# Optimization experiments

Hardware: AMD Instinct MI355X
Metric: run time of the kernel (lower is better)

The kernel has to match this reference:

```python
import jax, jax.numpy as jnp
import numpy as np

B, S, D_IN, HEAD_DIM = 4, 4096, 1024, 128

def setup_inputs() -> dict:
    key = jax.random.key(0)
    k1, k2, k3, k4 = jax.random.split(key, 4)
    x = jax.random.normal(k1, (B, S, D_IN), dtype=jnp.float32)
    # nn.Parameter(torch.rand(...)) -> uniform [0,1)
    W_query = jax.random.uniform(k2, (D_IN, HEAD_DIM), dtype=jnp.float32)
    W_key = jax.random.uniform(k3, (D_IN, HEAD_DIM), dtype=jnp.float32)
    W_value = jax.random.uniform(k4, (D_IN, HEAD_DIM), dtype=jnp.float32)
    return {"x": x, "W_query": W_query, "W_key": W_key, "W_value": W_value}

def reference(x, W_query, W_key, W_value):
    # x: [B,S,d_in]; W_*: [d_in,head_dim]
    queries = jnp.einsum('bsd,dh->bsh', x, W_query)
    keys = jnp.einsum('bsd,dh->bsh', x, W_key)
    values = jnp.einsum('bsd,dh->bsh', x, W_value)
    scale = 1.0 / jnp.sqrt(jnp.asarray(HEAD_DIM, dtype=x.dtype))
    attn_scores = jnp.einsum('bqh,bkh->bqk', queries, keys)  # [B,S,S]
    attn_weights = jax.nn.softmax(attn_scores * scale, axis=-1)
    context_vec = jnp.einsum('bqk,bkh->bqh', attn_weights, values)
    return context_vec
```

## Files before the change

### kernel.cpp

```cpp
#include <hip/hip_runtime.h>
#include <cstdint>

#define B_  4
#define S_  4096
#define DIN 1024
#define DH  128
#define QSCALE (0.08838834764831845f * 1.4426950408889634f)

typedef short bf16x8 __attribute__((ext_vector_type(8)));
typedef float f32x4 __attribute__((ext_vector_type(4)));
typedef unsigned short u16;
typedef unsigned int   u32;

#define MFMA16(a, b, c) __builtin_amdgcn_mfma_f32_16x16x32_bf16(a, b, c, 0, 0, 0)

#define GLOAD_LDS16(g, l) __builtin_amdgcn_global_load_lds( \
    (const __attribute__((address_space(1))) void*)(g),     \
    (__attribute__((address_space(3))) void*)(l), 16, 0, 0)

#if __has_builtin(__builtin_amdgcn_exp2f)
#define EXP2(x) __builtin_amdgcn_exp2f(x)
#else
#define EXP2(x) exp2f(x)
#endif

__device__ inline u16 bf16_rn(float f) {
    union { float f; u32 u; } v; v.f = f;
    u32 r = v.u + 0x7FFFu + ((v.u >> 16) & 1u);
    return (u16)(r >> 16);
}
__device__ inline float bf16_f(u16 h) {
    union { u32 u; float f; } v; v.u = ((u32)h) << 16; return v.f;
}
__device__ inline u32 pk2(float a, float b) {
    return (u32)bf16_rn(a) | ((u32)bf16_rn(b) << 16);
}
__device__ inline void split2(float a, float b, u32& hi, u32& lo) {
    u32 ua = __builtin_bit_cast(u32, a), ub = __builtin_bit_cast(u32, b);
    u32 ha = ua & 0xFFFF0000u, hb = ub & 0xFFFF0000u;
    hi = (ua >> 16) | hb;
    float la = a - __builtin_bit_cast(float, ha);
    float lb = b - __builtin_bit_cast(float, hb);
    lo = (u32)bf16_rn(la) | ((u32)bf16_rn(lb) << 16);
}

__global__ __launch_bounds__(256) void wconv2(
    const float* __restrict__ Wq, const float* __restrict__ Wk, const float* __restrict__ Wv,
    u16* __restrict__ wpack)
{
    int id  = blockIdx.x * 256 + threadIdx.x;
    int s   = id / 2560;
    int rem = id % 2560;
    int p   = rem >> 9;
    int gi  = rem & 511;
    int n   = gi & 127, kq2 = gi >> 7;
    const float* W = (p < 2) ? Wq : (p < 4) ? Wk : Wv;
    int k0 = 32 * s + 8 * kq2;
    u16 o[8];
    #pragma unroll
    for (int j = 0; j < 8; ++j) {
        float v = W[(size_t)(k0 + j) * DH + n];
        if (p < 2) v *= QSCALE;
        if (p == 4) {
            o[j] = bf16_rn(v);
        } else {
            u32 u = __builtin_bit_cast(u32, v);
            if ((p & 1) == 0) o[j] = (u16)(u >> 16);
            else o[j] = bf16_rn(v - __builtin_bit_cast(float, u & 0xFFFF0000u));
        }
    }
    u16* dst = wpack + (size_t)id * 8;
    *(uint4*)dst = *(uint4*)o;
}

__global__ __launch_bounds__(256, 2) void qkv_v5(
    const float* __restrict__ x, const u16* __restrict__ wpack,
    u16* __restrict__ qhi, u16* __restrict__ qlo,
    u16* __restrict__ khi, u16* __restrict__ klo, u16* __restrict__ vt)
{
    __shared__ __align__(16) char lds[65536];

    const int t    = threadIdx.x;
    const int row0 = blockIdx.x * 64;
    const int lane = t & 63, wave = t >> 6;
    const int l15  = lane & 15, g = lane >> 4;
    const int wr   = wave >> 1, wc = wave & 1;

    f32x4 accq[2][4], acck[2][4], accv[2][4];
    #pragma unroll
    for (int rt = 0; rt < 2; ++rt)
        #pragma unroll
        for (int nt = 0; nt < 4; ++nt)
            #pragma unroll
            for (int r = 0; r < 4; ++r) {
                accq[rt][nt][r] = 0.f; acck[rt][nt][r] = 0.f; accv[rt][nt][r] = 0.f;
            }

    const char* WP = (const char*)wpack;
    auto stage = [&](int bufi, int s) {
        char* d = lds + bufi * 32768;
        const char* src = WP + (size_t)s * 40960;
        #pragma unroll
        for (int c = 0; c < 8; ++c) {
            int o = t * 16 + c * 4096;
            GLOAD_LDS16(src + o, d + o);
        }
    };

    int wo_[4];
    #pragma unroll
    for (int nt = 0; nt < 4; ++nt)
        wo_[nt] = (g << 11) + ((64 * wc + 16 * nt + l15) << 4);

    const char* WV = WP + 32768;
    bf16x8 vcur[4], vnxt[4];
    #pragma unroll
    for (int nt = 0; nt < 4; ++nt)
        vcur[nt] = *(const bf16x8*)(WV + wo_[nt]);

    const float* xp0 = x + (size_t)(row0 + 32 * wr + l15) * DIN + 8 * g;
    const float* xp1 = xp0 + (size_t)16 * DIN;

    float4 ca0 = *(const float4*)(xp0);
    float4 cb0 = *(const float4*)(xp0 + 4);
    float4 ca1 = *(const float4*)(xp1);
    float4 cb1 = *(const float4*)(xp1 + 4);

    stage(0, 0);
    __syncthreads();

    int buf = 0;
    for (int s = 0; s < 32; ++s) {
        if (s < 31) stage(buf ^ 1, s + 1);

        float4 na0, nb0, na1, nb1;
        if (s < 31) {
            na0 = *(const float4*)(xp0 + 32 * (s + 1));
            nb0 = *(const float4*)(xp0 + 32 * (s + 1) + 4);
            na1 = *(const float4*)(xp1 + 32 * (s + 1));
            nb1 = *(const float4*)(xp1 + 32 * (s + 1) + 4);
            #pragma unroll
            for (int nt = 0; nt < 4; ++nt)
                vnxt[nt] = *(const bf16x8*)(WV + (size_t)(s + 1) * 40960 + wo_[nt]);
        }

        bf16x8 xh[2], xl[2];
        {
            uint4 H, L;
            split2(ca0.x, ca0.y, H.x, L.x); split2(ca0.z, ca0.w, H.y, L.y);
            split2(cb0.x, cb0.y, H.z, L.z); split2(cb0.z, cb0.w, H.w, L.w);
            xh[0] = __builtin_bit_cast(bf16x8, H);
            xl[0] = __builtin_bit_cast(bf16x8, L);
        }
        {
            uint4 H, L;
            split2(ca1.x, ca1.y, H.x, L.x); split2(ca1.z, ca1.w, H.y, L.y);
            split2(cb1.x, cb1.y, H.z, L.z); split2(cb1.z, cb1.w, H.w, L.w);
            xh[1] = __builtin_bit_cast(bf16x8, H);
            xl[1] = __builtin_bit_cast(bf16x8, L);
        }

        const char* wb = lds + buf * 32768;
        #pragma unroll
        for (int nt = 0; nt < 4; ++nt) {
            const int wo = wo_[nt];
            bf16x8 qwh = *(const bf16x8*)(wb + wo);
            bf16x8 qwl = *(const bf16x8*)(wb +  8192 + wo);
            bf16x8 kwh = *(const bf16x8*)(wb + 16384 + wo);
            bf16x8 kwl = *(const bf16x8*)(wb + 24576 + wo);
            #pragma unroll
            for (int rt = 0; rt < 2; ++rt) {
                accq[rt][nt] = MFMA16(xh[rt], qwh, accq[rt][nt]);
                accq[rt][nt] = MFMA16(xl[rt], qwh, accq[rt][nt]);
                accq[rt][nt] = MFMA16(xh[rt], qwl, accq[rt][nt]);
                acck[rt][nt] = MFMA16(xh[rt], kwh, acck[rt][nt]);
                acck[rt][nt] = MFMA16(xl[rt], kwh, acck[rt][nt]);
                acck[rt][nt] = MFMA16(xh[rt], kwl, acck[rt][nt]);
                accv[rt][nt] = MFMA16(xh[rt], vcur[nt], accv[rt][nt]);
            }
        }
        __syncthreads();
        if (s < 31) {
            ca0 = na0; cb0 = nb0; ca1 = na1; cb1 = nb1;
            #pragma unroll
            for (int nt = 0; nt < 4; ++nt) vcur[nt] = vnxt[nt];
        }
        buf ^= 1;
    }

    #pragma unroll
    for (int rt = 0; rt < 2; ++rt) {
        #pragma unroll
        for (int reg = 0; reg < 4; ++reg) {
            int r  = row0 + 32 * wr + 16 * rt + 4 * g + reg;
            int bb = r >> 12, sr = r & 4095, kt = sr >> 6, kr = sr & 63;
            #pragma unroll
            for (int nt = 0; nt < 4; ++nt) {
                int c = 64 * wc + 16 * nt + l15;
                {
                    float v = accq[rt][nt][reg];
                    u32 u = __builtin_bit_cast(u32, v);
                    float lo = v - __builtin_bit_cast(float, u & 0xFFFF0000u);
                    size_t o = (size_t)r * DH + c;
                    qhi[o] = (u16)(u >> 16);
                    qlo[o] = bf16_rn(lo);
                }
                {
                    float v = acck[rt][nt][reg];
                    u32 u = __builtin_bit_cast(u32, v);
                    float lo = v - __builtin_bit_cast(float, u & 0xFFFF0000u);
                    size_t o = ((size_t)(bb * 64 + kt) * 64 + kr) * 128
                             + (((c >> 3) ^ (kr & 15)) << 3) + (c & 7);
                    khi[o] = (u16)(u >> 16);
                    klo[o] = bf16_rn(lo);
                }
                {
                    float v = accv[rt][nt][reg];
                    size_t o = ((size_t)(bb * 64 + kt) * 128 + c) * 64
                             + (((kr >> 3) ^ (c & 7)) << 3) + (kr & 7);
                    vt[o] = bf16_rn(v);
                }
            }
        }
    }
}

__global__ __launch_bounds__(512, 2) void flash_db(
    const u16* __restrict__ qhi, const u16* __restrict__ qlo,
    const u16* __restrict__ khi, const u16* __restrict__ klo,
    const u16* __restrict__ vt,
    u16* __restrict__ opart, float2* __restrict__ ml)
{
    __shared__ __align__(16) char smem[2 * 49152];

    const int tid  = threadIdx.x;
    const int wave = tid >> 6, lane = tid & 63;
    const int l15  = lane & 15, g = lane >> 4;
    const int bid  = blockIdx.x;
    const int pair = bid & 15, qt = bid >> 4;
    const int b = pair >> 2, z = pair & 3;

    const int q0row = b * S_ + qt * 256 + wave * 32;

    bf16x8 qh[2][4], ql[2][4];
    #pragma unroll
    for (int h = 0; h < 2; ++h)
        #pragma unroll
        for (int ks = 0; ks < 4; ++ks) {
            size_t qa = (size_t)(q0row + 16 * h + l15) * DH + 32 * ks + 8 * g;
            qh[h][ks] = *(const bf16x8*)(qhi + qa);
            ql[h][ks] = *(const bf16x8*)(qlo + qa);
        }

    f32x4 O0[8], O1[8];
    #pragma unroll
    for (int dt = 0; dt < 8; ++dt)
        #pragma unroll
        for (int r = 0; r < 4; ++r) { O0[dt][r] = 0.f; O1[dt][r] = 0.f; }

    float m0 = -3.0e38f, l0 = 0.f, m1 = -3.0e38f, l1 = 0.f;

    int koff[4];
    #pragma unroll
    for (int ks = 0; ks < 4; ++ks)
        koff[ks] = (((4 * ks + g) ^ l15) << 4) + (l15 << 8);
    int voff[2];
    #pragma unroll
    for (int kw = 0; kw < 2; ++kw)
        voff[kw] = (((4 * kw + g) ^ (l15 & 7)) << 4);

    const char* kbase = (const char*)(khi + (size_t)b * 64 * 8192);
    const char* lbase = (const char*)(klo + (size_t)b * 64 * 8192);
    const char* vbase = (const char*)(vt  + (size_t)b * 64 * 8192);
    const int kt0 = z * 16;

    auto stage = [&](int bufi, int ktl) {
        const char* sk = kbase + (size_t)(kt0 + ktl) * 16384;
        const char* sl = lbase + (size_t)(kt0 + ktl) * 16384;
        const char* sv = vbase + (size_t)(kt0 + ktl) * 16384;
        char* dk = smem + bufi * 49152;
        #pragma unroll
        for (int c = 0; c < 2; ++c) {
            int o = tid * 16 + c * 8192;
            GLOAD_LDS16(sk + o, dk + o);
            GLOAD_LDS16(sl + o, dk + 16384 + o);
            GLOAD_LDS16(sv + o, dk + 32768 + o);
        }
    };

    stage(0, 0);
    __syncthreads();

    int buf = 0;
    for (int ktl = 0; ktl < 16; ++ktl) {
        if (ktl < 15) stage(buf ^ 1, ktl + 1);

        const char* bk = smem + buf * 49152;
        const char* bl = bk + 16384;
        const char* bv = bk + 32768;

        f32x4 s0[4], s1[4];
        #pragma unroll
        for (int nt = 0; nt < 4; ++nt)
            #pragma unroll
            for (int r = 0; r < 4; ++r) { s0[nt][r] = 0.f; s1[nt][r] = 0.f; }

        #pragma unroll
        for (int ks = 0; ks < 4; ++ks) {
            #pragma unroll
            for (int nt = 0; nt < 4; ++nt) {
                bf16x8 kh = *(const bf16x8*)(bk + nt * 4096 + koff[ks]);
                bf16x8 kl = *(const bf16x8*)(bl + nt * 4096 + koff[ks]);
                s0[nt] = MFMA16(kh, qh[0][ks], s0[nt]);
                s0[nt] = MFMA16(kh, ql[0][ks], s0[nt]);
                s0[nt] = MFMA16(kl, qh[0][ks], s0[nt]);
                s1[nt] = MFMA16(kh, qh[1][ks], s1[nt]);
                s1[nt] = MFMA16(kh, ql[1][ks], s1[nt]);
                s1[nt] = MFMA16(kl, qh[1][ks], s1[nt]);
            }
        }

        float ml0 = -3.0e38f, ml1 = -3.0e38f;
        #pragma unroll
        for (int nt = 0; nt < 4; ++nt)
            #pragma unroll
            for (int r = 0; r < 4; ++r) {
                ml0 = fmaxf(ml0, s0[nt][r]);
                ml1 = fmaxf(ml1, s1[nt][r]);
            }
        ml0 = fmaxf(ml0, __shfl_xor(ml0, 16));
        ml0 = fmaxf(ml0, __shfl_xor(ml0, 32));
        ml1 = fmaxf(ml1, __shfl_xor(ml1, 16));
        ml1 = fmaxf(ml1, __shfl_xor(ml1, 32));

        if (!__all((ml0 <= m0 + 8.0f) & (ml1 <= m1 + 8.0f))) {
            float mn0 = fmaxf(m0, ml0), mn1 = fmaxf(m1, ml1);
            float fsc0 = EXP2(m0 - mn0), fsc1 = EXP2(m1 - mn1);
            m0 = mn0; m1 = mn1;
            l0 *= fsc0; l1 *= fsc1;
            float fr0[4], fr1[4];
            #pragma unroll
            for (int r = 0; r < 4; ++r) {
                fr0[r] = __shfl(fsc0, 4 * g + r);
                fr1[r] = __shfl(fsc1, 4 * g + r);
            }
            #pragma unroll
            for (int dt = 0; dt < 8; ++dt)
                #pragma unroll
                for (int r = 0; r < 4; ++r) {
                    O0[dt][r] *= fr0[r];
                    O1[dt][r] *= fr1[r];
                }
        }

        u32 pk0[4][2], pk1[4][2];
        float ps0 = 0.f, ps1 = 0.f;
        #pragma unroll
        for (int nt = 0; nt < 4; ++nt) {
            float a0 = EXP2(s0[nt][0] - m0), a1 = EXP2(s0[nt][1] - m0);
            float a2 = EXP2(s0[nt][2] - m0), a3 = EXP2(s0[nt][3] - m0);
            ps0 += (a0 + a1) + (a2 + a3);
            pk0[nt][0] = pk2(a0, a1);
            pk0[nt][1] = pk2(a2, a3);
            float c0 = EXP2(s1[nt][0] - m1), c1 = EXP2(s1[nt][1] - m1);
            float c2 = EXP2(s1[nt][2] - m1), c3 = EXP2(s1[nt][3] - m1);
            ps1 += (c0 + c1) + (c2 + c3);
            pk1[nt][0] = pk2(c0, c1);
            pk1[nt][1] = pk2(c2, c3);
        }
        ps0 += __shfl_xor(ps0, 16);
        ps0 += __shfl_xor(ps0, 32);
        ps1 += __shfl_xor(ps1, 16);
        ps1 += __shfl_xor(ps1, 32);
        l0 += ps0; l1 += ps1;

        const int s0l = l15 | ((2 * (g & 1)) << 4);
        const int s1l = s0l + 16;
        const int hiH = g >> 1;
        #pragma unroll
        for (int kw = 0; kw < 2; ++kw) {
            u32 a0, a1, a2, a3, c0, c1, c2, c3;
            {
                u32 x0 = __shfl(pk0[2 * kw][0], s0l), y0 = __shfl(pk0[2 * kw + 1][0], s0l);
                u32 x1 = __shfl(pk0[2 * kw][1], s0l), y1 = __shfl(pk0[2 * kw + 1][1], s0l);
                u32 x2 = __shfl(pk0[2 * kw][0], s1l), y2 = __shfl(pk0[2 * kw + 1][0], s1l);
                u32 x3 = __shfl(pk0[2 * kw][1], s1l), y3 = __shfl(pk0[2 * kw + 1][1], s1l);
                a0 = hiH ? y0 : x0; a1 = hiH ? y1 : x1;
                a2 = hiH ? y2 : x2; a3 = hiH ? y3 : x3;
            }
            {
                u32 x0 = __shfl(pk1[2 * kw][0], s0l), y0 = __shfl(pk1[2 * kw + 1][0], s0l);
                u32 x1 = __shfl(pk1[2 * kw][1], s0l), y1 = __shfl(pk1[2 * kw + 1][1], s0l);
                u32 x2 = __shfl(pk1[2 * kw][0], s1l), y2 = __shfl(pk1[2 * kw + 1][0], s1l);
                u32 x3 = __shfl(pk1[2 * kw][1], s1l), y3 = __shfl(pk1[2 * kw + 1][1], s1l);
                c0 = hiH ? y0 : x0; c1 = hiH ? y1 : x1;
                c2 = hiH ? y2 : x2; c3 = hiH ? y3 : x3;
            }
            union { u32 w[4]; bf16x8 v; } pa, pb;
            pa.w[0] = a0; pa.w[1] = a1; pa.w[2] = a2; pa.w[3] = a3;
            pb.w[0] = c0; pb.w[1] = c1; pb.w[2] = c2; pb.w[3] = c3;
            #pragma unroll
            for (int dt = 0; dt < 8; ++dt) {
                bf16x8 vf = *(const bf16x8*)(bv + (16 * dt + l15) * 128 + voff[kw]);
                O0[dt] = MFMA16(pa.v, vf, O0[dt]);
                O1[dt] = MFMA16(pb.v, vf, O1[dt]);
            }
        }

        __syncthreads();
        buf ^= 1;
    }

    u16* op = opart + ((size_t)z * 16384 + q0row) * DH;
    #pragma unroll
    for (int dt = 0; dt < 8; ++dt)
        #pragma unroll
        for (int r = 0; r < 4; ++r) {
            op[(size_t)(4 * g + r) * DH + 16 * dt + l15]      = bf16_rn(O0[dt][r]);
            op[(size_t)(16 + 4 * g + r) * DH + 16 * dt + l15] = bf16_rn(O1[dt][r]);
        }
    if (lane < 16) {
        ml[(size_t)z * 16384 + q0row + lane]      = make_float2(m0, l0);
        ml[(size_t)z * 16384 + q0row + 16 + lane] = make_float2(m1, l1);
    }
}

__global__ __launch_bounds__(256) void merge4(
    const u16* __restrict__ op, const float2* __restrict__ ml, float* __restrict__ O)
{
    int row = blockIdx.x * 16 + (threadIdx.x >> 4);
    int dq  = (threadIdx.x & 15) * 8;
    float2 a[4];
    #pragma unroll
    for (int zz = 0; zz < 4; ++zz) a[zz] = ml[(size_t)zz * 16384 + row];
    float M = fmaxf(fmaxf(a[0].x, a[1].x), fmaxf(a[2].x, a[3].x));
    float w[4], den = 0.f;
    #pragma unroll
    for (int zz = 0; zz < 4; ++zz) {
        w[zz] = EXP2(a[zz].x - M);
        den += a[zz].y * w[zz];
    }
    float inv = 1.0f / den;
    float acc[8];
    #pragma unroll
    for (int j = 0; j < 8; ++j) acc[j] = 0.f;
    #pragma unroll
    for (int zz = 0; zz < 4; ++zz) {
        const u16* p = op + ((size_t)zz * 16384 + row) * DH + dq;
        bf16x8 vv = *(const bf16x8*)p;
        #pragma unroll
        for (int j = 0; j < 8; ++j) acc[j] += w[zz] * bf16_f((u16)vv[j]);
    }
    float4 oa, ob;
    oa.x = acc[0] * inv; oa.y = acc[1] * inv; oa.z = acc[2] * inv; oa.w = acc[3] * inv;
    ob.x = acc[4] * inv; ob.y = acc[5] * inv; ob.z = acc[6] * inv; ob.w = acc[7] * inv;
    *(float4*)(O + (size_t)row * DH + dq)     = oa;
    *(float4*)(O + (size_t)row * DH + dq + 4) = ob;
}

extern "C" void kernel_launch(void* const* d_in, const int* in_sizes, int n_in,
                              void* d_out, int out_size, void* d_ws, size_t ws_size,
                              hipStream_t stream) {
    const float* x  = (const float*)d_in[0];
    const float* Wq = (const float*)d_in[1];
    const float* Wk = (const float*)d_in[2];
    const float* Wv = (const float*)d_in[3];
    float* out = (float*)d_out;

    const size_t SZ = (size_t)B_ * S_ * DH;
    u16* qhi = (u16*)d_ws;
    u16* qlo = qhi + SZ;
    u16* khi = qlo + SZ;
    u16* klo = khi + SZ;
    u16* vtp = klo + SZ;
    u16* wpk = vtp + SZ;
    u16* opart = wpk + 655360;
    float2* mlp = (float2*)((char*)opart + (size_t)4 * 16384 * DH * 2);

    wconv2<<<320, 256, 0, stream>>>(Wq, Wk, Wv, wpk);
    qkv_v5<<<256, 256, 0, stream>>>(x, wpk, qhi, qlo, khi, klo, vtp);
    flash_db<<<256, 512, 0, stream>>>(qhi, qlo, khi, klo, vtp, opart, mlp);
    merge4<<<1024, 256, 0, stream>>>(opart, mlp, out);
}
```

Before: 150.9 us.

## Single-buffer QKV weight staging in LDS and load V weights from LDS

Replaces the double-buffered LDS weight pipeline in the QKV projection kernel with a single 40KB buffer staged each step, and moves the V-weight tile from direct global register prefetch into the same LDS stage. The x prefetch for the next step now issues after the barrier. This cuts LDS and register use, but it gives up the overlap between staging the next weight slice and running the MFMAs on the current one, so each step now waits on its own staging load.

Result: faster. 145.2 us (-3.8%).

```diff
diff --git a/kernel.cpp b/kernel.cpp
--- a/kernel.cpp
+++ b/kernel.cpp
@@ -73,12 +73,12 @@
     *(uint4*)dst = *(uint4*)o;
 }
 
-__global__ __launch_bounds__(256, 2) void qkv_v5(
+__global__ __launch_bounds__(256) void qkv_v6(
     const float* __restrict__ x, const u16* __restrict__ wpack,
     u16* __restrict__ qhi, u16* __restrict__ qlo,
     u16* __restrict__ khi, u16* __restrict__ klo, u16* __restrict__ vt)
 {
-    __shared__ __align__(16) char lds[65536];
+    __shared__ __align__(16) char lds[40960];
 
     const int t    = threadIdx.x;
     const int row0 = blockIdx.x * 64;
@@ -97,26 +97,14 @@
             }
 
     const char* WP = (const char*)wpack;
-    auto stage = [&](int bufi, int s) {
-        char* d = lds + bufi * 32768;
+    auto stage = [&](int s) {
         const char* src = WP + (size_t)s * 40960;
         #pragma unroll
-        for (int c = 0; c < 8; ++c) {
+        for (int c = 0; c < 10; ++c) {
             int o = t * 16 + c * 4096;
-            GLOAD_LDS16(src + o, d + o);
+            GLOAD_LDS16(src + o, lds + o);
         }
     };
-
-    int wo_[4];
-    #pragma unroll
-    for (int nt = 0; nt < 4; ++nt)
-        wo_[nt] = (g << 11) + ((64 * wc + 16 * nt + l15) << 4);
-
-    const char* WV = WP + 32768;
-    bf16x8 vcur[4], vnxt[4];
-    #pragma unroll
-    for (int nt = 0; nt < 4; ++nt)
-        vcur[nt] = *(const bf16x8*)(WV + wo_[nt]);
 
     const float* xp0 = x + (size_t)(row0 + 32 * wr + l15) * DIN + 8 * g;
     const float* xp1 = xp0 + (size_t)16 * DIN;
@@ -126,23 +114,8 @@
     float4 ca1 = *(const float4*)(xp1);
     float4 cb1 = *(const float4*)(xp1 + 4);
 
-    stage(0, 0);
-    __syncthreads();
-
-    int buf = 0;
     for (int s = 0; s < 32; ++s) {
-        if (s < 31) stage(buf ^ 1, s + 1);
-
-        float4 na0, nb0, na1, nb1;
-        if (s < 31) {
-            na0 = *(const float4*)(xp0 + 32 * (s + 1));
-            nb0 = *(const float4*)(xp0 + 32 * (s + 1) + 4);
-            na1 = *(const float4*)(xp1 + 32 * (s + 1));
-            nb1 = *(const float4*)(xp1 + 32 * (s + 1) + 4);
-            #pragma unroll
-            for (int nt = 0; nt < 4; ++nt)
-                vnxt[nt] = *(const bf16x8*)(WV + (size_t)(s + 1) * 40960 + wo_[nt]);
-        }
+        stage(s);
 
         bf16x8 xh[2], xl[2];
         {
@@ -160,14 +133,25 @@
             xl[1] = __builtin_bit_cast(bf16x8, L);
         }
 
-        const char* wb = lds + buf * 32768;
+        __syncthreads();
+
+        float4 na0, nb0, na1, nb1;
+        if (s < 31) {
+            na0 = *(const float4*)(xp0 + 32 * (s + 1));
+            nb0 = *(const float4*)(xp0 + 32 * (s + 1) + 4);
+            na1 = *(const float4*)(xp1 + 32 * (s + 1));
+            nb1 = *(const float4*)(xp1 + 32 * (s + 1) + 4);
+        }
+
         #pragma unroll
         for (int nt = 0; nt < 4; ++nt) {
-            const int wo = wo_[nt];
-            bf16x8 qwh = *(const bf16x8*)(wb + wo);
-            bf16x8 qwl = *(const bf16x8*)(wb +  8192 + wo);
-            bf16x8 kwh = *(const bf16x8*)(wb + 16384 + wo);
-            bf16x8 kwl = *(const bf16x8*)(wb + 24576 + wo);
+            const int n  = 64 * wc + 16 * nt + l15;
+            const int wo = (g << 11) + (n << 4);
+            bf16x8 qwh = *(const bf16x8*)(lds + wo);
+            bf16x8 qwl = *(const bf16x8*)(lds +  8192 + wo);
+            bf16x8 kwh = *(const bf16x8*)(lds + 16384 + wo);
+            bf16x8 kwl = *(const bf16x8*)(lds + 24576 + wo);
+            bf16x8 vwh = *(const bf16x8*)(lds + 32768 + wo);
             #pragma unroll
             for (int rt = 0; rt < 2; ++rt) {
                 accq[rt][nt] = MFMA16(xh[rt], qwh, accq[rt][nt]);
@@ -176,16 +160,11 @@
                 acck[rt][nt] = MFMA16(xh[rt], kwh, acck[rt][nt]);
                 acck[rt][nt] = MFMA16(xl[rt], kwh, acck[rt][nt]);
                 acck[rt][nt] = MFMA16(xh[rt], kwl, acck[rt][nt]);
-                accv[rt][nt] = MFMA16(xh[rt], vcur[nt], accv[rt][nt]);
+                accv[rt][nt] = MFMA16(xh[rt], vwh, accv[rt][nt]);
             }
         }
         __syncthreads();
-        if (s < 31) {
-            ca0 = na0; cb0 = nb0; ca1 = na1; cb1 = nb1;
-            #pragma unroll
-            for (int nt = 0; nt < 4; ++nt) vcur[nt] = vnxt[nt];
-        }
-        buf ^= 1;
+        if (s < 31) { ca0 = na0; cb0 = nb0; ca1 = na1; cb1 = nb1; }
     }
 
     #pragma unroll
@@ -478,7 +457,7 @@
     float2* mlp = (float2*)((char*)opart + (size_t)4 * 16384 * DH * 2);
 
     wconv2<<<320, 256, 0, stream>>>(Wq, Wk, Wv, wpk);
-    qkv_v5<<<256, 256, 0, stream>>>(x, wpk, qhi, qlo, khi, klo, vtp);
+    qkv_v6<<<256, 256, 0, stream>>>(x, wpk, qhi, qlo, khi, klo, vtp);
     flash_db<<<256, 512, 0, stream>>>(qhi, qlo, khi, klo, vtp, opart, mlp);
     merge4<<<1024, 256, 0, stream>>>(opart, mlp, out);
 }
```
